# Kernel tuning notes

Measured on AMD Instinct MI355X. Metric: run time of the kernel, lower is better.

Reference implementation:

```python
import jax, jax.numpy as jnp
import numpy as np

B, H, S, D = 2, 12, 2048, 64


def setup_inputs() -> dict:
    key = jax.random.key(0)
    kq, kk, kv = jax.random.split(key, 3)
    q = jax.random.normal(kq, (B, H, S, D), dtype=jnp.float32)
    k = jax.random.normal(kk, (B, H, S, D), dtype=jnp.float32)
    v = jax.random.normal(kv, (B, H, S, D), dtype=jnp.float32)
    # causal mask: True = attend (keep), lower triangle
    mask = jnp.tril(jnp.ones((S, S), dtype=bool))
    return {"q": q, "k": k, "v": v, "mask": mask}


def reference(q, k, v, mask):
    dim = q.shape[-1]
    # [B,H,S,S] scores
    scores = jnp.einsum("bhqd,bhkd->bhqk", q, k) / jnp.sqrt(jnp.asarray(dim, q.dtype))
    # dynamic mask-direction logic from the original module:
    # if the mask is denser in the strict upper triangle, True means "mask out";
    # otherwise True means "keep".
    sq = mask.shape[-1]
    sample = mask.reshape(-1, sq, sq)[0]
    upper = jnp.triu(jnp.ones_like(sample, dtype=bool), k=1)
    flip = jnp.sum(sample & upper) > jnp.sum(sample & ~upper)
    keep = jnp.where(flip, ~mask, mask)  # True = keep
    neg_inf = jnp.asarray(-jnp.inf, scores.dtype)
    scores = jnp.where(keep, scores, neg_inf)
    weights = jax.nn.softmax(scores, axis=-1)
    # dropout with p_drop=0.0 is the identity
    return jnp.einsum("bhqk,bhkd->bhqd", weights, v)
```

## Files before the change

kernel.cpp:

```cpp
#include <hip/hip_runtime.h>
#include <hip/hip_bf16.h>


#define SEQ 2048
#define DH 64
#define NHEADS 24
#define BN 64
#define LDK 72
#define NSLOT (NHEADS * 16 * 4)
#define WS_FA14  ((size_t)NSLOT * 8192 * 2 + (size_t)NSLOT * 128 * 4)

typedef float f32x4 __attribute__((ext_vector_type(4)));
typedef float f32x16 __attribute__((ext_vector_type(16)));
typedef __bf16 bf16x8 __attribute__((ext_vector_type(8)));
typedef __bf16 bf16x4 __attribute__((ext_vector_type(4)));
typedef unsigned int u32;
typedef u32 u32x4 __attribute__((ext_vector_type(4)));
typedef unsigned short u16;

#if __has_builtin(__builtin_amdgcn_exp2f)
#define EXP2F(x) __builtin_amdgcn_exp2f(x)
#else
#define EXP2F(x) exp2f(x)
#endif

#define QSCALE 0.1803368801111204f

static __device__ __forceinline__ u32 pk2(float a, float b) {
    u16 ua = __builtin_bit_cast(u16, (__bf16)a);
    u16 ub = __builtin_bit_cast(u16, (__bf16)b);
    return (u32)ua | ((u32)ub << 16);
}

__global__ __launch_bounds__(256, 3)
void fa21_kernel(const float* __restrict__ q, const float* __restrict__ k,
                 const float* __restrict__ v,
                 __bf16* __restrict__ opart, float* __restrict__ lpart,
                 float* __restrict__ out)
{
    const int bx = blockIdx.x;
    const int xcd = bx & 7;
    const int sub = bx >> 3;
    const int bh = (sub / 40) * 8 + xcd;
    const int rem = 39 - (sub % 40);
    int mt2, st;
    if      (rem >= 36) { mt2 = 15; st = 36; }
    else if (rem >= 32) { mt2 = 14; st = 32; }
    else if (rem >= 28) { mt2 = 13; st = 28; }
    else if (rem >= 24) { mt2 = 12; st = 24; }
    else if (rem >= 21) { mt2 = 11; st = 21; }
    else if (rem >= 18) { mt2 = 10; st = 18; }
    else if (rem >= 15) { mt2 = 9;  st = 15; }
    else if (rem >= 12) { mt2 = 8;  st = 12; }
    else if (rem >= 10) { mt2 = 7;  st = 10; }
    else if (rem >= 8)  { mt2 = 6;  st = 8; }
    else if (rem >= 6)  { mt2 = 5;  st = 6; }
    else if (rem >= 4)  { mt2 = 4;  st = 4; }
    else                { mt2 = rem; st = rem; }
    const int chunk = rem - st;
    const int jt0 = chunk * 8;
    const int jt_end = min(jt0 + 8, 2 * mt2 + 2);
    const int q0 = mt2 * 128;

    const int tid = threadIdx.x;
    const int w = tid >> 6, lane = tid & 63;
    const int l31 = lane & 31;
    const int hb = lane >> 5;

    __shared__ __bf16 Ks[2][4096];
    __shared__ __bf16 Vs[2][4096];

    const float* kh = k + (size_t)bh * SEQ * DH;
    const float* vh = v + (size_t)bh * SEQ * DH;
    const int qg = q0 + w * 32 + l31;

    bf16x8 qn[4];
    {
        const float* qp = q + (size_t)bh * SEQ * DH + (size_t)qg * DH + hb * 8;
        #pragma unroll
        for (int ks = 0; ks < 4; ++ks) {
            f32x4 x0 = *(const f32x4*)(qp + 16 * ks);
            f32x4 x1 = *(const f32x4*)(qp + 16 * ks + 4);
            #pragma unroll
            for (int j = 0; j < 4; ++j) {
                qn[ks][j]     = (__bf16)(x0[j] * QSCALE);
                qn[ks][4 + j] = (__bf16)(x1[j] * QSCALE);
            }
        }
    }

    f32x16 acc_o0 = {}, acc_o1 = {};
    float lsum = 0.0f;

    const int srow0 = tid >> 3;
    const int sg    = tid & 7;
    const int klg   = sg ^ (srow0 & 7);

    const int kb    = (tid & 7) * 4 + ((tid & 128) >> 2);
    const int kb2   = (kb & ~0xC) | ((kb & 4) << 1) | ((kb & 8) >> 1);
    const int dbase = ((tid >> 3) & 15) * 4;

    f32x4 ka[2][2], va[4];
    auto issueKV = [&](int jt) {
        const float* kp = kh + (size_t)(jt * BN + srow0) * DH + klg * 8;
        ka[0][0] = *(const f32x4*)kp;
        ka[0][1] = *(const f32x4*)(kp + 4);
        kp += 32 * DH;
        ka[1][0] = *(const f32x4*)kp;
        ka[1][1] = *(const f32x4*)(kp + 4);
        const float* vpx = vh + (size_t)(jt * BN + kb2) * DH + dbase;
        #pragma unroll
        for (int ii = 0; ii < 4; ++ii) va[ii] = *(const f32x4*)(vpx + ii * DH);
    };
    auto commitKV = [&](int b) {
        #pragma unroll
        for (int s = 0; s < 2; ++s) {
            bf16x8 o;
            #pragma unroll
            for (int jj = 0; jj < 4; ++jj) {
                o[jj]     = (__bf16)ka[s][0][jj];
                o[4 + jj] = (__bf16)ka[s][1][jj];
            }
            *(bf16x8*)((char*)Ks[b] + s * 4096 + tid * 16) = o;
        }
        #pragma unroll
        for (int dd = 0; dd < 4; ++dd) {
            const int d = dbase + dd;
            bf16x4 p4v;
            #pragma unroll
            for (int ii = 0; ii < 4; ++ii) p4v[ii] = (__bf16)va[ii][dd];
            *(bf16x4*)((char*)Vs[b] + d * 128 +
                       ((((kb >> 3) ^ (d & 7)) << 4) | ((kb & 7) * 2))) = p4v;
        }
    };

    issueKV(jt0);
    commitKV(0);
    if (jt0 + 1 < jt_end) issueKV(jt0 + 1);
    __syncthreads();

    int buf = 0;
    for (int jt = jt0; jt < jt_end; ++jt) {
        if (jt + 1 < jt_end) commitKV(buf ^ 1);
        if (jt + 2 < jt_end) issueKV(jt + 2);

        const char* Kb = (const char*)Ks[buf];
        const char* Vb = (const char*)Vs[buf];
        f32x16 sa0 = {}, sa1 = {};
        __builtin_amdgcn_s_setprio(1);
        #pragma unroll
        for (int ks = 0; ks < 4; ++ks) {
            bf16x8 kf0 = *(const bf16x8*)(Kb + l31 * 128 +
                                          (((2 * ks + hb) ^ (lane & 7)) << 4));
            bf16x8 kf1 = *(const bf16x8*)(Kb + (32 + l31) * 128 +
                                          (((2 * ks + hb) ^ (lane & 7)) << 4));
            sa0 = __builtin_amdgcn_mfma_f32_32x32x16_bf16(kf0, qn[ks], sa0, 0, 0, 0);
            sa1 = __builtin_amdgcn_mfma_f32_32x32x16_bf16(kf1, qn[ks], sa1, 0, 0, 0);
        }
        __builtin_amdgcn_s_setprio(0);

        if (jt >= 2 * mt2) {
            #pragma unroll
            for (int reg = 0; reg < 16; ++reg) {
                const int kvr = jt * 64 + (reg & 3) + 8 * (reg >> 2) + 4 * hb;
                if (kvr > qg)      sa0[reg] = -1e30f;
                if (kvr + 32 > qg) sa1[reg] = -1e30f;
            }
        }

        u32 pk[8][2];
        #pragma unroll
        for (int sp = 0; sp < 4; ++sp) {
            float e0 = EXP2F(sa0[4 * sp + 0]), e1 = EXP2F(sa0[4 * sp + 1]);
            float e2 = EXP2F(sa0[4 * sp + 2]), e3 = EXP2F(sa0[4 * sp + 3]);
            float f0 = EXP2F(sa1[4 * sp + 0]), f1 = EXP2F(sa1[4 * sp + 1]);
            float f2 = EXP2F(sa1[4 * sp + 2]), f3 = EXP2F(sa1[4 * sp + 3]);
            lsum += ((e0 + e1) + (e2 + e3)) + ((f0 + f1) + (f2 + f3));
            pk[sp][0]     = pk2(e0, e1); pk[sp][1]     = pk2(e2, e3);
            pk[4 + sp][0] = pk2(f0, f1); pk[4 + sp][1] = pk2(f2, f3);
        }

        __builtin_amdgcn_s_setprio(1);
        #pragma unroll
        for (int s = 0; s < 4; ++s) {
            u32x4 uv;
            uv[0] = pk[2 * s][0];
            uv[1] = pk[2 * s][1];
            uv[2] = pk[2 * s + 1][0];
            uv[3] = pk[2 * s + 1][1];
            bf16x8 pf = __builtin_bit_cast(bf16x8, uv);
            bf16x8 vf0 = *(const bf16x8*)(Vb + l31 * 128 +
                                          (((2 * s + hb) ^ (lane & 7)) << 4));
            bf16x8 vf1 = *(const bf16x8*)(Vb + (32 + l31) * 128 +
                                          (((2 * s + hb) ^ (lane & 7)) << 4));
            acc_o0 = __builtin_amdgcn_mfma_f32_32x32x16_bf16(pf, vf0, acc_o0, 0, 0, 0);
            acc_o1 = __builtin_amdgcn_mfma_f32_32x32x16_bf16(pf, vf1, acc_o1, 0, 0, 0);
        }
        __builtin_amdgcn_s_setprio(0);

        if (jt + 1 < jt_end) __syncthreads();
        buf ^= 1;
    }

    const float ltot = lsum + __shfl_xor(lsum, 32, 64);

    if (2 * mt2 + 2 <= 8) {
        float* oh = out + (size_t)bh * SEQ * DH;
        #pragma unroll
        for (int reg = 0; reg < 16; ++reg) {
            const int rr = (reg & 3) + 8 * (reg >> 2) + 4 * hb;
            const float lr = __shfl(ltot, rr, 64);
            const float inv = 1.0f / lr;
            const int row = q0 + w * 32 + rr;
            oh[(size_t)row * DH + l31]      = acc_o0[reg] * inv;
            oh[(size_t)row * DH + 32 + l31] = acc_o1[reg] * inv;
        }
    } else {
        const int slot = (bh * 16 + mt2) * 4 + chunk;
        __bf16* po = opart + (size_t)slot * 8192;
        #pragma unroll
        for (int reg = 0; reg < 16; ++reg) {
            const int row = w * 32 + (reg & 3) + 8 * (reg >> 2) + 4 * hb;
            po[row * 64 + l31]      = (__bf16)acc_o0[reg];
            po[row * 64 + 32 + l31] = (__bf16)acc_o1[reg];
        }
        if (hb == 0) lpart[(size_t)slot * 128 + w * 32 + l31] = ltot;
    }
}

__global__ __launch_bounds__(256)
void fa_reduce(const __bf16* __restrict__ opart, const float* __restrict__ lpart,
               float* __restrict__ out)
{
    const int bx = blockIdx.x;
    const int xcd = bx & 7;
    const int r2 = bx >> 3;
    const int bh = (r2 / 12) * 8 + xcd;
    const int mt2 = 4 + (r2 % 12);
    const int nc = (mt2 >> 2) + 1;
    const int base = (bh * 16 + mt2) * 4;
    const int tid = threadIdx.x;
    #pragma unroll
    for (int rnd = 0; rnd < 8; ++rnd) {
        const int flat = rnd * 1024 + tid * 4;
        const int row = flat >> 6;
        float o0 = 0, o1 = 0, o2 = 0, o3 = 0, l = 0;
        for (int c = 0; c < nc; ++c) {
            bf16x4 ov = *(const bf16x4*)(opart + (size_t)(base + c) * 8192 + flat);
            o0 += (float)ov[0]; o1 += (float)ov[1]; o2 += (float)ov[2]; o3 += (float)ov[3];
            l += lpart[(size_t)(base + c) * 128 + row];
        }
        const float inv = 1.0f / l;
        f32x4 res = { o0 * inv, o1 * inv, o2 * inv, o3 * inv };
        *(f32x4*)(out + (size_t)bh * SEQ * DH + (size_t)mt2 * 8192 + flat) = res;
    }
}

__global__ __launch_bounds__(256, 2)
void fa_causal_kernel(const float* __restrict__ q, const float* __restrict__ k,
                      const float* __restrict__ v, float* __restrict__ out)
{
    const int mt = 31 - (blockIdx.x & 31);
    const int bh = blockIdx.x >> 5;
    const int tid = threadIdx.x;
    const int w = tid >> 6, lane = tid & 63;
    const int g = lane >> 4, li = lane & 15;
    const int m0 = mt * 64;
    __shared__ __bf16 KsF[BN][LDK];
    __shared__ __bf16 VsF[DH][LDK];
    __shared__ __bf16 PsF[4][16][LDK];
    const size_t head_off = (size_t)bh * SEQ * DH;
    const float* qh = q + head_off;
    const float* kh = k + head_off;
    const float* vh = v + head_off;
    float* oh = out + head_off;
    const int qrow = m0 + w * 16 + li;
    bf16x8 qf[2];
    {
        const float* qp = qh + (size_t)qrow * DH + g * 8;
        #pragma unroll
        for (int c = 0; c < 2; ++c) {
            const float* p = qp + c * 32;
            #pragma unroll
            for (int jj = 0; jj < 8; ++jj) qf[c][jj] = (__bf16)p[jj];
        }
    }
    f32x4 acc[4] = {};
    float mrow[4], lrow[4];
    #pragma unroll
    for (int r = 0; r < 4; ++r) { mrow[r] = -1e30f; lrow[r] = 0.0f; }
    const float scale = 0.125f;
    const int srow = tid >> 2, scol = (tid & 3) * 16;
    for (int jt = 0; jt <= mt; ++jt) {
        const int kv0 = jt * BN;
        __syncthreads();
        {
            const float* kp = kh + (size_t)(kv0 + srow) * DH + scol;
            __bf16 tmp[16];
            #pragma unroll
            for (int jj = 0; jj < 16; ++jj) tmp[jj] = (__bf16)kp[jj];
            *(bf16x8*)&KsF[srow][scol]     = *(bf16x8*)&tmp[0];
            *(bf16x8*)&KsF[srow][scol + 8] = *(bf16x8*)&tmp[8];
            const float* vp = vh + (size_t)(kv0 + srow) * DH + scol;
            #pragma unroll
            for (int jj = 0; jj < 16; ++jj) VsF[scol + jj][srow] = (__bf16)vp[jj];
        }
        __syncthreads();
        float s4[4][4];
        #pragma unroll
        for (int t = 0; t < 4; ++t) {
            f32x4 sa = {};
            #pragma unroll
            for (int c = 0; c < 2; ++c) {
                bf16x8 kfr = *(const bf16x8*)&KsF[t * 16 + li][c * 32 + g * 8];
                sa = __builtin_amdgcn_mfma_f32_16x16x32_bf16(qf[c], kfr, sa, 0, 0, 0);
            }
            #pragma unroll
            for (int r = 0; r < 4; ++r) s4[t][r] = sa[r] * scale;
        }
        if (jt == mt) {
            #pragma unroll
            for (int t = 0; t < 4; ++t) {
                const int col = kv0 + t * 16 + li;
                #pragma unroll
                for (int r = 0; r < 4; ++r)
                    if (col > m0 + w * 16 + g * 4 + r) s4[t][r] = -1e30f;
            }
        }
        #pragma unroll
        for (int r = 0; r < 4; ++r) {
            float mx = fmaxf(fmaxf(s4[0][r], s4[1][r]), fmaxf(s4[2][r], s4[3][r]));
            #pragma unroll
            for (int off = 1; off < 16; off <<= 1)
                mx = fmaxf(mx, __shfl_xor(mx, off, 64));
            const float mnew = fmaxf(mrow[r], mx);
            const float alpha = __expf(mrow[r] - mnew);
            mrow[r] = mnew;
            float ps = 0.0f;
            #pragma unroll
            for (int t = 0; t < 4; ++t) {
                const float p = __expf(s4[t][r] - mnew);
                s4[t][r] = p;
                ps += p;
            }
            #pragma unroll
            for (int off = 1; off < 16; off <<= 1)
                ps += __shfl_xor(ps, off, 64);
            lrow[r] = lrow[r] * alpha + ps;
            #pragma unroll
            for (int t = 0; t < 4; ++t) acc[t][r] *= alpha;
        }
        #pragma unroll
        for (int t = 0; t < 4; ++t)
            #pragma unroll
            for (int r = 0; r < 4; ++r)
                PsF[w][g * 4 + r][t * 16 + li] = (__bf16)s4[t][r];
        __syncthreads();
        #pragma unroll
        for (int c = 0; c < 2; ++c) {
            bf16x8 pf = *(const bf16x8*)&PsF[w][li][c * 32 + g * 8];
            #pragma unroll
            for (int t = 0; t < 4; ++t) {
                bf16x8 vfr = *(const bf16x8*)&VsF[t * 16 + li][c * 32 + g * 8];
                acc[t] = __builtin_amdgcn_mfma_f32_16x16x32_bf16(pf, vfr, acc[t], 0, 0, 0);
            }
        }
    }
    #pragma unroll
    for (int r = 0; r < 4; ++r) {
        const int row = m0 + w * 16 + g * 4 + r;
        const float inv = 1.0f / lrow[r];
        float* op = oh + (size_t)row * DH + li;
        #pragma unroll
        for (int t = 0; t < 4; ++t) op[t * 16] = acc[t][r] * inv;
    }
}

extern "C" void kernel_launch(void* const* d_in, const int* in_sizes, int n_in,
                              void* d_out, int out_size, void* d_ws, size_t ws_size,
                              hipStream_t stream) {
    (void)in_sizes; (void)n_in; (void)out_size;
    const float* q = (const float*)d_in[0];
    const float* k = (const float*)d_in[1];
    const float* v = (const float*)d_in[2];
    float* out = (float*)d_out;

    if (ws_size >= WS_FA14) {
        __bf16* opart = (__bf16*)d_ws;
        float* lpart = (float*)((char*)d_ws + (size_t)NSLOT * 8192 * 2);
        fa21_kernel<<<dim3(960), dim3(256), 0, stream>>>(q, k, v, opart, lpart, out);
        fa_reduce<<<dim3(288), dim3(256), 0, stream>>>(opart, lpart, out);
    } else {
        fa_causal_kernel<<<dim3(NHEADS * 32), dim3(256), 0, stream>>>(q, k, v, out);
    }
}
```

Before: 129.7 us.

## Drop split-KV partial outputs and reduce pass; one block per query tile

Each 128-row query tile is now handled by a single block that walks its entire causal KV range. This replaces the 960-block split-KV launch, the bf16 partial-output workspace and the separate reduce kernel. The intent is to remove the extra launch, the workspace traffic and the reduction. The cost is a much longer serial KV loop for the last query tiles, with only 384 blocks to spread the causal triangle's uneven work. The small-workspace fallback kernel is also removed.

```diff
diff --git a/kernel.cpp b/kernel.cpp
--- a/kernel.cpp
+++ b/kernel.cpp
@@ -6,9 +6,6 @@
 #define DH 64
 #define NHEADS 24
 #define BN 64
-#define LDK 72
-#define NSLOT (NHEADS * 16 * 4)
-#define WS_FA14  ((size_t)NSLOT * 8192 * 2 + (size_t)NSLOT * 128 * 4)
 
 typedef float f32x4 __attribute__((ext_vector_type(4)));
 typedef float f32x16 __attribute__((ext_vector_type(16)));
@@ -33,33 +30,15 @@
 }
 
 __global__ __launch_bounds__(256, 3)
-void fa21_kernel(const float* __restrict__ q, const float* __restrict__ k,
-                 const float* __restrict__ v,
-                 __bf16* __restrict__ opart, float* __restrict__ lpart,
-                 float* __restrict__ out)
+void fa22_kernel(const float* __restrict__ q, const float* __restrict__ k,
+                 const float* __restrict__ v, float* __restrict__ out)
 {
     const int bx = blockIdx.x;
     const int xcd = bx & 7;
     const int sub = bx >> 3;
-    const int bh = (sub / 40) * 8 + xcd;
-    const int rem = 39 - (sub % 40);
-    int mt2, st;
-    if      (rem >= 36) { mt2 = 15; st = 36; }
-    else if (rem >= 32) { mt2 = 14; st = 32; }
-    else if (rem >= 28) { mt2 = 13; st = 28; }
-    else if (rem >= 24) { mt2 = 12; st = 24; }
-    else if (rem >= 21) { mt2 = 11; st = 21; }
-    else if (rem >= 18) { mt2 = 10; st = 18; }
-    else if (rem >= 15) { mt2 = 9;  st = 15; }
-    else if (rem >= 12) { mt2 = 8;  st = 12; }
-    else if (rem >= 10) { mt2 = 7;  st = 10; }
-    else if (rem >= 8)  { mt2 = 6;  st = 8; }
-    else if (rem >= 6)  { mt2 = 5;  st = 6; }
-    else if (rem >= 4)  { mt2 = 4;  st = 4; }
-    else                { mt2 = rem; st = rem; }
-    const int chunk = rem - st;
-    const int jt0 = chunk * 8;
-    const int jt_end = min(jt0 + 8, 2 * mt2 + 2);
+    const int bh = (sub >> 4) * 8 + xcd;
+    const int mt2 = 15 - (sub & 15);
+    const int jt_end = 2 * mt2 + 2;
     const int q0 = mt2 * 128;
 
     const int tid = threadIdx.x;
@@ -134,13 +113,13 @@
         }
     };
 
-    issueKV(jt0);
+    issueKV(0);
     commitKV(0);
-    if (jt0 + 1 < jt_end) issueKV(jt0 + 1);
+    if (1 < jt_end) issueKV(1);
     __syncthreads();
 
     int buf = 0;
-    for (int jt = jt0; jt < jt_end; ++jt) {
+    for (int jt = 0; jt < jt_end; ++jt) {
         if (jt + 1 < jt_end) commitKV(buf ^ 1);
         if (jt + 2 < jt_end) issueKV(jt + 2);
 
@@ -204,193 +183,26 @@
 
     const float ltot = lsum + __shfl_xor(lsum, 32, 64);
 
-    if (2 * mt2 + 2 <= 8) {
-        float* oh = out + (size_t)bh * SEQ * DH;
-        #pragma unroll
-        for (int reg = 0; reg < 16; ++reg) {
-            const int rr = (reg & 3) + 8 * (reg >> 2) + 4 * hb;
-            const float lr = __shfl(ltot, rr, 64);
-            const float inv = 1.0f / lr;
-            const int row = q0 + w * 32 + rr;
-            oh[(size_t)row * DH + l31]      = acc_o0[reg] * inv;
-            oh[(size_t)row * DH + 32 + l31] = acc_o1[reg] * inv;
-        }
-    } else {
-        const int slot = (bh * 16 + mt2) * 4 + chunk;
-        __bf16* po = opart + (size_t)slot * 8192;
-        #pragma unroll
-        for (int reg = 0; reg < 16; ++reg) {
-            const int row = w * 32 + (reg & 3) + 8 * (reg >> 2) + 4 * hb;
-            po[row * 64 + l31]      = (__bf16)acc_o0[reg];
-            po[row * 64 + 32 + l31] = (__bf16)acc_o1[reg];
-        }
-        if (hb == 0) lpart[(size_t)slot * 128 + w * 32 + l31] = ltot;
-    }
-}
-
-__global__ __launch_bounds__(256)
-void fa_reduce(const __bf16* __restrict__ opart, const float* __restrict__ lpart,
-               float* __restrict__ out)
-{
-    const int bx = blockIdx.x;
-    const int xcd = bx & 7;
-    const int r2 = bx >> 3;
-    const int bh = (r2 / 12) * 8 + xcd;
-    const int mt2 = 4 + (r2 % 12);
-    const int nc = (mt2 >> 2) + 1;
-    const int base = (bh * 16 + mt2) * 4;
-    const int tid = threadIdx.x;
+    float* oh = out + (size_t)bh * SEQ * DH;
     #pragma unroll
-    for (int rnd = 0; rnd < 8; ++rnd) {
-        const int flat = rnd * 1024 + tid * 4;
-        const int row = flat >> 6;
-        float o0 = 0, o1 = 0, o2 = 0, o3 = 0, l = 0;
-        for (int c = 0; c < nc; ++c) {
-            bf16x4 ov = *(const bf16x4*)(opart + (size_t)(base + c) * 8192 + flat);
-            o0 += (float)ov[0]; o1 += (float)ov[1]; o2 += (float)ov[2]; o3 += (float)ov[3];
-            l += lpart[(size_t)(base + c) * 128 + row];
-        }
-        const float inv = 1.0f / l;
-        f32x4 res = { o0 * inv, o1 * inv, o2 * inv, o3 * inv };
-        *(f32x4*)(out + (size_t)bh * SEQ * DH + (size_t)mt2 * 8192 + flat) = res;
-    }
-}
-
-__global__ __launch_bounds__(256, 2)
-void fa_causal_kernel(const float* __restrict__ q, const float* __restrict__ k,
-                      const float* __restrict__ v, float* __restrict__ out)
-{
-    const int mt = 31 - (blockIdx.x & 31);
-    const int bh = blockIdx.x >> 5;
-    const int tid = threadIdx.x;
-    const int w = tid >> 6, lane = tid & 63;
-    const int g = lane >> 4, li = lane & 15;
-    const int m0 = mt * 64;
-    __shared__ __bf16 KsF[BN][LDK];
-    __shared__ __bf16 VsF[DH][LDK];
-    __shared__ __bf16 PsF[4][16][LDK];
-    const size_t head_off = (size_t)bh * SEQ * DH;
-    const float* qh = q + head_off;
-    const float* kh = k + head_off;
-    const float* vh = v + head_off;
-    float* oh = out + head_off;
-    const int qrow = m0 + w * 16 + li;
-    bf16x8 qf[2];
-    {
-        const float* qp = qh + (size_t)qrow * DH + g * 8;
-        #pragma unroll
-        for (int c = 0; c < 2; ++c) {
-            const float* p = qp + c * 32;
-            #pragma unroll
-            for (int jj = 0; jj < 8; ++jj) qf[c][jj] = (__bf16)p[jj];
-        }
-    }
-    f32x4 acc[4] = {};
-    float mrow[4], lrow[4];
-    #pragma unroll
-    for (int r = 0; r < 4; ++r) { mrow[r] = -1e30f; lrow[r] = 0.0f; }
-    const float scale = 0.125f;
-    const int srow = tid >> 2, scol = (tid & 3) * 16;
-    for (int jt = 0; jt <= mt; ++jt) {
-        const int kv0 = jt * BN;
-        __syncthreads();
-        {
-            const float* kp = kh + (size_t)(kv0 + srow) * DH + scol;
-            __bf16 tmp[16];
-            #pragma unroll
-            for (int jj = 0; jj < 16; ++jj) tmp[jj] = (__bf16)kp[jj];
-            *(bf16x8*)&KsF[srow][scol]     = *(bf16x8*)&tmp[0];
-            *(bf16x8*)&KsF[srow][scol + 8] = *(bf16x8*)&tmp[8];
-            const float* vp = vh + (size_t)(kv0 + srow) * DH + scol;
-            #pragma unroll
-            for (int jj = 0; jj < 16; ++jj) VsF[scol + jj][srow] = (__bf16)vp[jj];
-        }
-        __syncthreads();
-        float s4[4][4];
-        #pragma unroll
-        for (int t = 0; t < 4; ++t) {
-            f32x4 sa = {};
-            #pragma unroll
-            for (int c = 0; c < 2; ++c) {
-                bf16x8 kfr = *(const bf16x8*)&KsF[t * 16 + li][c * 32 + g * 8];
-                sa = __builtin_amdgcn_mfma_f32_16x16x32_bf16(qf[c], kfr, sa, 0, 0, 0);
-            }
-            #pragma unroll
-            for (int r = 0; r < 4; ++r) s4[t][r] = sa[r] * scale;
-        }
-        if (jt == mt) {
-            #pragma unroll
-            for (int t = 0; t < 4; ++t) {
-                const int col = kv0 + t * 16 + li;
-                #pragma unroll
-                for (int r = 0; r < 4; ++r)
-                    if (col > m0 + w * 16 + g * 4 + r) s4[t][r] = -1e30f;
-            }
-        }
-        #pragma unroll
-        for (int r = 0; r < 4; ++r) {
-            float mx = fmaxf(fmaxf(s4[0][r], s4[1][r]), fmaxf(s4[2][r], s4[3][r]));
-            #pragma unroll
-            for (int off = 1; off < 16; off <<= 1)
-                mx = fmaxf(mx, __shfl_xor(mx, off, 64));
-            const float mnew = fmaxf(mrow[r], mx);
-            const float alpha = __expf(mrow[r] - mnew);
-            mrow[r] = mnew;
-            float ps = 0.0f;
-            #pragma unroll
-            for (int t = 0; t < 4; ++t) {
-                const float p = __expf(s4[t][r] - mnew);
-                s4[t][r] = p;
-                ps += p;
-            }
-            #pragma unroll
-            for (int off = 1; off < 16; off <<= 1)
-                ps += __shfl_xor(ps, off, 64);
-            lrow[r] = lrow[r] * alpha + ps;
-            #pragma unroll
-            for (int t = 0; t < 4; ++t) acc[t][r] *= alpha;
-        }
-        #pragma unroll
-        for (int t = 0; t < 4; ++t)
-            #pragma unroll
-            for (int r = 0; r < 4; ++r)
-                PsF[w][g * 4 + r][t * 16 + li] = (__bf16)s4[t][r];
-        __syncthreads();
-        #pragma unroll
-        for (int c = 0; c < 2; ++c) {
-            bf16x8 pf = *(const bf16x8*)&PsF[w][li][c * 32 + g * 8];
-            #pragma unroll
-            for (int t = 0; t < 4; ++t) {
-                bf16x8 vfr = *(const bf16x8*)&VsF[t * 16 + li][c * 32 + g * 8];
-                acc[t] = __builtin_amdgcn_mfma_f32_16x16x32_bf16(pf, vfr, acc[t], 0, 0, 0);
-            }
-        }
-    }
-    #pragma unroll
-    for (int r = 0; r < 4; ++r) {
-        const int row = m0 + w * 16 + g * 4 + r;
-        const float inv = 1.0f / lrow[r];
-        float* op = oh + (size_t)row * DH + li;
-        #pragma unroll
-        for (int t = 0; t < 4; ++t) op[t * 16] = acc[t][r] * inv;
+    for (int reg = 0; reg < 16; ++reg) {
+        const int rr = (reg & 3) + 8 * (reg >> 2) + 4 * hb;
+        const float lr = __shfl(ltot, rr, 64);
+        const float inv = 1.0f / lr;
+        const int row = q0 + w * 32 + rr;
+        oh[(size_t)row * DH + l31]      = acc_o0[reg] * inv;
+        oh[(size_t)row * DH + 32 + l31] = acc_o1[reg] * inv;
     }
 }
 
 extern "C" void kernel_launch(void* const* d_in, const int* in_sizes, int n_in,
                               void* d_out, int out_size, void* d_ws, size_t ws_size,
                               hipStream_t stream) {
-    (void)in_sizes; (void)n_in; (void)out_size;
+    (void)in_sizes; (void)n_in; (void)out_size; (void)d_ws; (void)ws_size;
     const float* q = (const float*)d_in[0];
     const float* k = (const float*)d_in[1];
     const float* v = (const float*)d_in[2];
     float* out = (float*)d_out;
 
-    if (ws_size >= WS_FA14) {
-        __bf16* opart = (__bf16*)d_ws;
-        float* lpart = (float*)((char*)d_ws + (size_t)NSLOT * 8192 * 2);
-        fa21_kernel<<<dim3(960), dim3(256), 0, stream>>>(q, k, v, opart, lpart, out);
-        fa_reduce<<<dim3(288), dim3(256), 0, stream>>>(opart, lpart, out);
-    } else {
-        fa_causal_kernel<<<dim3(NHEADS * 32), dim3(256), 0, stream>>>(q, k, v, out);
-    }
+    fa22_kernel<<<dim3(384), dim3(256), 0, stream>>>(q, k, v, out);
 }
```

Measured after the change: 132.0 us. No clear change (+1.8%).
